# Optimization experiments

Measured on AMD Instinct MI355X. Metric: run time of the kernel, lower is better.

The kernel has to match this reference:

```python
import jax, jax.numpy as jnp
import numpy as np

N = 4096
DIMS = {"word": 768, "pos": 64, "liwc": 93, "entity": 256, "text": 768}
HID, OUT = 256, 128
VIEWS = ["word", "pos", "liwc", "entity", "text"]


def setup_inputs() -> dict:
    key = jax.random.key(0)
    inp = {}
    for i, v in enumerate(VIEWS):
        ka, kx, k1, k2 = jax.random.split(jax.random.fold_in(key, i), 4)
        d = DIMS[v]
        # dense row-normalized adjacency surrogate
        a = jax.random.uniform(ka, (N, N), dtype=jnp.float32)
        inp[f"adj_{v}"] = a / jnp.sum(a, axis=1, keepdims=True)
        inp[f"x_{v}"] = jax.random.normal(kx, (N, d), dtype=jnp.float32)
        inp[f"W1_{v}"] = jax.random.normal(k1, (d, HID), dtype=jnp.float32) * (2.0 / (d + HID)) ** 0.5
        inp[f"b1_{v}"] = jnp.zeros((HID,), dtype=jnp.float32)
        inp[f"W2_{v}"] = jax.random.normal(k2, (HID, OUT), dtype=jnp.float32) * (2.0 / (HID + OUT)) ** 0.5
        inp[f"b2_{v}"] = jnp.zeros((OUT,), dtype=jnp.float32)
    return inp


def _gcn2(adj, x, W1, b1, W2, b2):
    # layer 1: adj @ (x @ W1) + b1, relu (dropout is identity in eval mode)
    h = jax.nn.relu(adj @ (x @ W1) + b1)
    # layer 2
    return adj @ (h @ W2) + b2


def reference(adj_word, adj_pos, adj_liwc, adj_entity, adj_text,
              x_word, x_pos, x_liwc, x_entity, x_text,
              W1_word, b1_word, W2_word, b2_word,
              W1_pos, b1_pos, W2_pos, b2_pos,
              W1_liwc, b1_liwc, W2_liwc, b2_liwc,
              W1_entity, b1_entity, W2_entity, b2_entity,
              W1_text, b1_text, W2_text, b2_text):
    return (
        _gcn2(adj_word, x_word, W1_word, b1_word, W2_word, b2_word),
        _gcn2(adj_pos, x_pos, W1_pos, b1_pos, W2_pos, b2_pos),
        _gcn2(adj_liwc, x_liwc, W1_liwc, b1_liwc, W2_liwc, b2_liwc),
        _gcn2(adj_entity, x_entity, W1_entity, b1_entity, W2_entity, b2_entity),
        _gcn2(adj_text, x_text, W1_text, b1_text, W2_text, b2_text),
    )
```

## Files before the change

kernel.cpp:

```cpp
#include <hip/hip_runtime.h>
#include <stdint.h>

typedef unsigned short u16;
typedef __attribute__((ext_vector_type(8))) __bf16 bf16x8;
typedef __attribute__((ext_vector_type(4))) float f32x4;
typedef __attribute__((ext_vector_type(4))) u16 u16x4;
typedef __attribute__((ext_vector_type(8))) u16 u16x8;

#define BM 128
#define BN 128
#define BK 32
#define MTOT 4096

__device__ __forceinline__ u16 f2bf(float f) {
  union { float f; uint32_t u; } x; x.f = f;
  uint32_t r = x.u + 0x7FFFu + ((x.u >> 16) & 1u);
  return (u16)(r >> 16);
}
__device__ __forceinline__ float bf2f(u16 h) {
  union { uint32_t u; float f; } x; x.u = ((uint32_t)h) << 16;
  return x.f;
}

__device__ __forceinline__ void gload16(const void* g, void* lds) {
  __builtin_amdgcn_global_load_lds(
      (const __attribute__((address_space(1))) void*)g,
      (__attribute__((address_space(3))) void*)lds, 16, 0, 0);
}

struct ViewParams {
  const void* A;
  const u16* BT;
  void* C;
  const float* bias;
  int ldab, lda, N;
  int kspan;
  size_t partStride;
};
struct Params5 { ViewParams v[5]; };

template <int FLAGS, bool AF32, bool CF32>
__global__ __launch_bounds__(256) void gemm_kernel(Params5 p, int tilesPerView,
                                                   int ntiles, int kchunks) {
  constexpr int ABYTES = AF32 ? (BM * BK * 4) : (BM * BK * 2);
  __shared__ __align__(16) char smem[ABYTES + BN * BK * 2];
  u16* Bs = (u16*)(smem + ABYTES);

  const int bid = blockIdx.x;
  const int view = bid / tilesPerView;
  const int t = bid - view * tilesPerView;
  const int kc = t % kchunks;
  const int t2 = t / kchunks;
  const int nt = t2 % ntiles;
  const int mt = t2 / ntiles;
  ViewParams vp = p.v[view];
  const int ldab = vp.ldab, lda = vp.lda, N = vp.N;
  const int m0 = mt * BM, n0 = nt * BN;
  const int kbase = kc * vp.kspan;

  const int tid = threadIdx.x;
  const int wave = tid >> 6;
  const int lane = tid & 63;

  const int srow = lane >> 2;
  const int slot4 = lane & 3;
  const int rB0 = wave * 32 + srow;
  const int rB1 = rB0 + 16;
  const int cB0 = slot4 ^ ((rB0 >> 1) & 3);
  const int cB1 = slot4 ^ ((rB1 >> 1) & 3);
  const u16* gB0 = vp.BT + (size_t)(n0 + rB0) * ldab + kbase + cB0 * 8;
  const u16* gB1 = vp.BT + (size_t)(n0 + rB1) * ldab + kbase + cB1 * 8;
  u16* lB0 = Bs + (wave * 32) * 32;
  u16* lB1 = Bs + (wave * 32 + 16) * 32;

  const float* gAf[4];
  float* lAf[4];
  const u16 *gAb0 = nullptr, *gAb1 = nullptr;
  u16 *lAb0 = nullptr, *lAb1 = nullptr;
  if constexpr (AF32) {
    const float* Af = (const float*)vp.A;
    const int arow = lane >> 3;
    const int slot8 = lane & 7;
#pragma unroll
    for (int i = 0; i < 4; i++) {
      int r = wave * 32 + i * 8 + arow;
      int c = slot8 ^ (r & 7);
      gAf[i] = Af + (size_t)(m0 + r) * lda + kbase + c * 4;
      lAf[i] = (float*)smem + (wave * 32 + i * 8) * 32;
    }
  } else {
    const u16* Ab = (const u16*)vp.A;
    const int rA0 = wave * 32 + srow;
    const int rA1 = rA0 + 16;
    const int cA0 = slot4 ^ ((rA0 >> 1) & 3);
    const int cA1 = slot4 ^ ((rA1 >> 1) & 3);
    gAb0 = Ab + (size_t)(m0 + rA0) * lda + kbase + cA0 * 8;
    gAb1 = Ab + (size_t)(m0 + rA1) * lda + kbase + cA1 * 8;
    lAb0 = (u16*)smem + (wave * 32) * 32;
    lAb1 = (u16*)smem + (wave * 32 + 16) * 32;
  }

  const int lm = lane & 15;
  const int q = lane >> 4;
  const int wm = (wave >> 1) * 64;
  const int wn = (wave & 1) * 64;
  int aoff0[4], aoff1[4], boff[4];
#pragma unroll
  for (int i = 0; i < 4; i++) {
    int ml = wm + i * 16 + lm;
    if constexpr (AF32) {
      aoff0[i] = ml * 32 + ((2 * q) ^ (ml & 7)) * 4;
      aoff1[i] = ml * 32 + ((2 * q + 1) ^ (ml & 7)) * 4;
    } else {
      aoff0[i] = ml * 32 + (q ^ ((ml >> 1) & 3)) * 8;
    }
    int nl = wn + i * 16 + lm;
    boff[i] = nl * 32 + (q ^ ((nl >> 1) & 3)) * 8;
  }

  f32x4 acc[4][4];
#pragma unroll
  for (int i = 0; i < 4; i++)
#pragma unroll
    for (int j = 0; j < 4; j++) acc[i][j] = 0.0f;

  for (int ks = 0; ks < vp.kspan; ks += BK) {
    if constexpr (AF32) {
#pragma unroll
      for (int i = 0; i < 4; i++) { gload16(gAf[i], lAf[i]); gAf[i] += BK; }
    } else {
      gload16(gAb0, lAb0); gload16(gAb1, lAb1);
      gAb0 += BK; gAb1 += BK;
    }
    gload16(gB0, lB0); gload16(gB1, lB1);
    gB0 += BK; gB1 += BK;
    __syncthreads();

    bf16x8 af[4], bfr[4];
#pragma unroll
    for (int i = 0; i < 4; i++) {
      if constexpr (AF32) {
        f32x4 lo = *(const f32x4*)((const float*)smem + aoff0[i]);
        f32x4 hi = *(const f32x4*)((const float*)smem + aoff1[i]);
        bf16x8 a;
#pragma unroll
        for (int tt = 0; tt < 4; tt++) { a[tt] = (__bf16)lo[tt]; a[tt + 4] = (__bf16)hi[tt]; }
        af[i] = a;
      } else {
        af[i] = *(const bf16x8*)((const u16*)smem + aoff0[i]);
      }
    }
#pragma unroll
    for (int j = 0; j < 4; j++) bfr[j] = *(const bf16x8*)(Bs + boff[j]);
#pragma unroll
    for (int i = 0; i < 4; i++)
#pragma unroll
      for (int j = 0; j < 4; j++)
        acc[i][j] = __builtin_amdgcn_mfma_f32_16x16x32_bf16(af[i], bfr[j], acc[i][j], 0, 0, 0);
    __syncthreads();
  }

#pragma unroll
  for (int j = 0; j < 4; j++) {
    const int n = n0 + wn + j * 16 + lm;
    float bv = 0.0f;
    if (FLAGS & 2) bv = vp.bias[n];
#pragma unroll
    for (int i = 0; i < 4; i++) {
      const int mb = m0 + wm + i * 16 + q * 4;
      float v0 = acc[i][j][0], v1 = acc[i][j][1], v2 = acc[i][j][2], v3 = acc[i][j][3];
      if (FLAGS & 2) { v0 += bv; v1 += bv; v2 += bv; v3 += bv; }
      if (FLAGS & 4) {
        v0 = fmaxf(v0, 0.0f); v1 = fmaxf(v1, 0.0f);
        v2 = fmaxf(v2, 0.0f); v3 = fmaxf(v3, 0.0f);
      }
      if constexpr ((FLAGS & 1) != 0) {
        u16x4 pk;
        pk[0] = f2bf(v0); pk[1] = f2bf(v1); pk[2] = f2bf(v2); pk[3] = f2bf(v3);
        *(u16x4*)((u16*)vp.C + (size_t)kc * vp.partStride + (size_t)n * MTOT + mb) = pk;
      } else if constexpr (CF32) {
        float* cp = (float*)vp.C + (size_t)kc * vp.partStride + (size_t)mb * N + n;
        cp[0] = v0; cp[N] = v1; cp[2 * N] = v2; cp[3 * N] = v3;
      } else {
        u16* cp = (u16*)vp.C + (size_t)kc * vp.partStride + (size_t)mb * N + n;
        cp[0] = f2bf(v0); cp[N] = f2bf(v1); cp[2 * N] = f2bf(v2); cp[3 * N] = f2bf(v3);
      }
    }
  }
}

struct CombParams { const u16* parts; u16* out; const float* b[5]; int kchunks; };
__global__ __launch_bounds__(256) void comb_h_kernel(CombParams cp) {
  int idx = blockIdx.x * 256 + threadIdx.x;
  int v = idx >> 17;
  int e = (idx & 131071) << 3;
  float acc[8] = {0, 0, 0, 0, 0, 0, 0, 0};
  for (int kc = 0; kc < cp.kchunks; kc++) {
    u16x8 t = *(const u16x8*)(cp.parts + (((size_t)(kc * 5 + v)) << 20) + e);
#pragma unroll
    for (int j = 0; j < 8; j++) acc[j] += bf2f(t[j]);
  }
  const float* bp = cp.b[v] + (e & 255);
  u16x8 o;
#pragma unroll
  for (int j = 0; j < 8; j++) o[j] = f2bf(fmaxf(acc[j] + bp[j], 0.0f));
  *(u16x8*)(cp.out + (((size_t)v) << 20) + e) = o;
}

struct CombFParams { const float* parts; float* out; const float* b[5]; int kchunks; };
__global__ __launch_bounds__(256) void combf_kernel(CombFParams cp) {
  int idx = blockIdx.x * 256 + threadIdx.x;
  int v = idx >> 16;
  int e = (idx & 65535) << 3;
  float acc[8] = {0, 0, 0, 0, 0, 0, 0, 0};
  for (int kc = 0; kc < cp.kchunks; kc++) {
    const float* pp = cp.parts + (((size_t)(kc * 5 + v)) << 19) + e;
    f32x4 a = *(const f32x4*)pp;
    f32x4 b = *(const f32x4*)(pp + 4);
#pragma unroll
    for (int j = 0; j < 4; j++) { acc[j] += a[j]; acc[j + 4] += b[j]; }
  }
  const float* bp = cp.b[v] + (e & 127);
  f32x4 o0, o1;
#pragma unroll
  for (int j = 0; j < 4; j++) { o0[j] = acc[j] + bp[j]; o1[j] = acc[j + 4] + bp[j + 4]; }
  float* op = cp.out + (((size_t)v) << 19) + e;
  *(f32x4*)op = o0;
  *(f32x4*)(op + 4) = o1;
}

struct PrepParams {
  const float* W1[5]; u16* W1T[5];
  const float* W2[5]; u16* W2T[5];
  const float* xl; float* xlp;
  int d[5]; int Kp[5];
};

__global__ void prep_kernel(PrepParams p, int total) {
  int idx = blockIdx.x * 256 + threadIdx.x;
  if (idx >= total) return;
  int off = 0;
#pragma unroll
  for (int v = 0; v < 5; v++) {
    int sz = 256 * p.Kp[v];
    if (idx < off + sz) {
      int r = idx - off;
      int n = r / p.Kp[v];
      int k = r - n * p.Kp[v];
      p.W1T[v][r] = (k < p.d[v]) ? f2bf(p.W1[v][(size_t)k * 256 + n]) : (u16)0;
      return;
    }
    off += sz;
  }
#pragma unroll
  for (int v = 0; v < 5; v++) {
    if (idx < off + 128 * 256) {
      int r = idx - off;
      int n = r >> 8, k = r & 255;
      p.W2T[v][r] = f2bf(p.W2[v][(size_t)k * 128 + n]);
      return;
    }
    off += 128 * 256;
  }
  {
    int r = idx - off;
    int m = r / 96, k = r - m * 96;
    p.xlp[r] = (k < 93) ? p.xl[(size_t)m * 93 + k] : 0.0f;
  }
}

extern "C" void kernel_launch(void* const* d_in, const int* in_sizes, int n_in,
                              void* d_out, int out_size, void* d_ws, size_t ws_size,
                              hipStream_t stream) {
  (void)in_sizes; (void)n_in; (void)out_size;
  static const int dims[5] = {768, 64, 93, 256, 768};
  static const int Kp[5]   = {768, 64, 96, 256, 768};

  const float *adjf[5], *xf[5], *W1f[5], *b1f[5], *W2f[5], *b2f[5];
  for (int v = 0; v < 5; v++) {
    adjf[v] = (const float*)d_in[6 * v + 0];
    xf[v]   = (const float*)d_in[6 * v + 1];
    W1f[v]  = (const float*)d_in[6 * v + 2];
    b1f[v]  = (const float*)d_in[6 * v + 3];
    W2f[v]  = (const float*)d_in[6 * v + 4];
    b2f[v]  = (const float*)d_in[6 * v + 5];
  }

  const size_t VIEW = (size_t)256 * 4096;
  const size_t TV   = (size_t)128 * 4096;
  char* ws = (char*)d_ws;
  size_t off = 0;
  auto carve = [&](size_t bytes) { char* pp = ws + off; off += (bytes + 15) & ~(size_t)15; return pp; };
  u16* W1T[5]; for (int v = 0; v < 5; v++) W1T[v] = (u16*)carve((size_t)256 * Kp[v] * 2);
  u16* W2T[5]; for (int v = 0; v < 5; v++) W2T[v] = (u16*)carve((size_t)128 * 256 * 2);
  float* xlp = (float*)carve((size_t)4096 * 96 * 4);
  u16* Y1T = (u16*)carve(5 * VIEW * 2);
  u16* PARTS = (u16*)carve(2 * 5 * VIEW * 2);
  u16* HT = (u16*)carve(5 * VIEW * 2);
  const bool ksplit = ws_size >= off;
  u16* TT = Y1T;
  float* PARTSF = (float*)PARTS;

  PrepParams pp;
  int prepTot = 0;
  for (int v = 0; v < 5; v++) {
    pp.W1[v] = W1f[v]; pp.W1T[v] = W1T[v];
    pp.W2[v] = W2f[v]; pp.W2T[v] = W2T[v];
    pp.d[v] = dims[v]; pp.Kp[v] = Kp[v];
    prepTot += 256 * Kp[v];
  }
  pp.xl = xf[2]; pp.xlp = xlp;
  prepTot += 5 * 128 * 256 + 4096 * 96;
  prep_kernel<<<(prepTot + 255) / 256, 256, 0, stream>>>(pp, prepTot);

  Params5 pa;
  for (int v = 0; v < 5; v++)
    pa.v[v] = ViewParams{ (v == 2 ? (const void*)xlp : (const void*)xf[v]), W1T[v], Y1T + v * VIEW,
                          nullptr, Kp[v], Kp[v], 256, Kp[v], 0 };
  gemm_kernel<1, true, false><<<320, 256, 0, stream>>>(pa, 64, 2, 1);

  if (ksplit) {
    Params5 pb;
    for (int v = 0; v < 5; v++)
      pb.v[v] = ViewParams{ adjf[v], Y1T + v * VIEW, PARTS + v * VIEW,
                            nullptr, 4096, 4096, 256, 2048, 5 * VIEW };
    gemm_kernel<0, true, false><<<640, 256, 0, stream>>>(pb, 128, 2, 2);

    CombParams c1{ PARTS, HT, { b1f[0], b1f[1], b1f[2], b1f[3], b1f[4] }, 2 };
    comb_h_kernel<<<2560, 256, 0, stream>>>(c1);

    Params5 pc;
    for (int v = 0; v < 5; v++)
      pc.v[v] = ViewParams{ HT + v * VIEW, W2T[v], TT + v * TV,
                            nullptr, 256, 256, 128, 256, 0 };
    gemm_kernel<1, false, false><<<160, 256, 0, stream>>>(pc, 32, 1, 1);

    Params5 pd;
    for (int v = 0; v < 5; v++)
      pd.v[v] = ViewParams{ adjf[v], TT + v * TV, PARTSF + v * TV,
                            nullptr, 4096, 4096, 128, 2048, 5 * TV };
    gemm_kernel<0, true, true><<<320, 256, 0, stream>>>(pd, 64, 1, 2);

    CombFParams c2{ PARTSF, (float*)d_out, { b2f[0], b2f[1], b2f[2], b2f[3], b2f[4] }, 2 };
    combf_kernel<<<1280, 256, 0, stream>>>(c2);
  } else {
    Params5 pb;
    for (int v = 0; v < 5; v++)
      pb.v[v] = ViewParams{ adjf[v], Y1T + v * VIEW, HT + v * VIEW,
                            b1f[v], 4096, 4096, 256, 4096, 0 };
    gemm_kernel<6, true, false><<<320, 256, 0, stream>>>(pb, 64, 2, 1);

    Params5 pc;
    for (int v = 0; v < 5; v++)
      pc.v[v] = ViewParams{ HT + v * VIEW, W2T[v], TT + v * TV,
                            nullptr, 256, 256, 128, 256, 0 };
    gemm_kernel<1, false, false><<<160, 256, 0, stream>>>(pc, 32, 1, 1);

    Params5 pd;
    float* outp = (float*)d_out;
    for (int v = 0; v < 5; v++)
      pd.v[v] = ViewParams{ adjf[v], TT + v * TV, outp + v * TV,
                            b2f[v], 4096, 4096, 128, 4096, 0 };
    gemm_kernel<2, true, true><<<160, 256, 0, stream>>>(pd, 32, 1, 1);
  }
}
```

Measured before the change: 579.4 us.

## Double-buffer LDS tiles to overlap global loads with MFMA compute

Doubles the shared-memory footprint into two ping-pong buffers, so the next K-slice is issued with async global-to-LDS loads while MFMAs run on the current slice. This removes one of the two barriers per iteration and hides part of the global load latency behind compute. In exchange LDS use doubles, which may lower occupancy, especially for the fp32-A variant. It also depends on the barrier correctly covering completion of the async direct-to-LDS loads.

```diff
diff --git a/kernel.cpp b/kernel.cpp
--- a/kernel.cpp
+++ b/kernel.cpp
@@ -43,8 +43,8 @@
 __global__ __launch_bounds__(256) void gemm_kernel(Params5 p, int tilesPerView,
                                                    int ntiles, int kchunks) {
   constexpr int ABYTES = AF32 ? (BM * BK * 4) : (BM * BK * 2);
-  __shared__ __align__(16) char smem[ABYTES + BN * BK * 2];
-  u16* Bs = (u16*)(smem + ABYTES);
+  constexpr int BUFB = ABYTES + BN * BK * 2;
+  __shared__ __align__(16) char smem[2 * BUFB];
 
   const int bid = blockIdx.x;
   const int view = bid / tilesPerView;
@@ -70,13 +70,12 @@
   const int cB1 = slot4 ^ ((rB1 >> 1) & 3);
   const u16* gB0 = vp.BT + (size_t)(n0 + rB0) * ldab + kbase + cB0 * 8;
   const u16* gB1 = vp.BT + (size_t)(n0 + rB1) * ldab + kbase + cB1 * 8;
-  u16* lB0 = Bs + (wave * 32) * 32;
-  u16* lB1 = Bs + (wave * 32 + 16) * 32;
+  const int lB0_off = ABYTES + (wave * 32) * 32 * 2;
+  const int lB1_off = ABYTES + (wave * 32 + 16) * 32 * 2;
 
   const float* gAf[4];
-  float* lAf[4];
   const u16 *gAb0 = nullptr, *gAb1 = nullptr;
-  u16 *lAb0 = nullptr, *lAb1 = nullptr;
+  int lA_off[4];
   if constexpr (AF32) {
     const float* Af = (const float*)vp.A;
     const int arow = lane >> 3;
@@ -86,7 +85,7 @@
       int r = wave * 32 + i * 8 + arow;
       int c = slot8 ^ (r & 7);
       gAf[i] = Af + (size_t)(m0 + r) * lda + kbase + c * 4;
-      lAf[i] = (float*)smem + (wave * 32 + i * 8) * 32;
+      lA_off[i] = (wave * 32 + i * 8) * 32 * 4;
     }
   } else {
     const u16* Ab = (const u16*)vp.A;
@@ -96,8 +95,8 @@
     const int cA1 = slot4 ^ ((rA1 >> 1) & 3);
     gAb0 = Ab + (size_t)(m0 + rA0) * lda + kbase + cA0 * 8;
     gAb1 = Ab + (size_t)(m0 + rA1) * lda + kbase + cA1 * 8;
-    lAb0 = (u16*)smem + (wave * 32) * 32;
-    lAb1 = (u16*)smem + (wave * 32 + 16) * 32;
+    lA_off[0] = (wave * 32) * 32 * 2;
+    lA_off[1] = (wave * 32 + 16) * 32 * 2;
   }
 
   const int lm = lane & 15;
@@ -124,32 +123,36 @@
 #pragma unroll
     for (int j = 0; j < 4; j++) acc[i][j] = 0.0f;
 
-  for (int ks = 0; ks < vp.kspan; ks += BK) {
+  auto stage = [&](char* bufp) {
     if constexpr (AF32) {
 #pragma unroll
-      for (int i = 0; i < 4; i++) { gload16(gAf[i], lAf[i]); gAf[i] += BK; }
+      for (int i = 0; i < 4; i++) { gload16(gAf[i], bufp + lA_off[i]); gAf[i] += BK; }
     } else {
-      gload16(gAb0, lAb0); gload16(gAb1, lAb1);
+      gload16(gAb0, bufp + lA_off[0]);
+      gload16(gAb1, bufp + lA_off[1]);
       gAb0 += BK; gAb1 += BK;
     }
-    gload16(gB0, lB0); gload16(gB1, lB1);
+    gload16(gB0, bufp + lB0_off);
+    gload16(gB1, bufp + lB1_off);
     gB0 += BK; gB1 += BK;
-    __syncthreads();
-
+  };
+
+  auto compute = [&](const char* bufp) {
     bf16x8 af[4], bfr[4];
 #pragma unroll
     for (int i = 0; i < 4; i++) {
       if constexpr (AF32) {
-        f32x4 lo = *(const f32x4*)((const float*)smem + aoff0[i]);
-        f32x4 hi = *(const f32x4*)((const float*)smem + aoff1[i]);
+        f32x4 lo = *(const f32x4*)((const float*)bufp + aoff0[i]);
+        f32x4 hi = *(const f32x4*)((const float*)bufp + aoff1[i]);
         bf16x8 a;
 #pragma unroll
         for (int tt = 0; tt < 4; tt++) { a[tt] = (__bf16)lo[tt]; a[tt + 4] = (__bf16)hi[tt]; }
         af[i] = a;
       } else {
-        af[i] = *(const bf16x8*)((const u16*)smem + aoff0[i]);
+        af[i] = *(const bf16x8*)((const u16*)bufp + aoff0[i]);
       }
     }
+    const u16* Bs = (const u16*)(bufp + ABYTES);
 #pragma unroll
     for (int j = 0; j < 4; j++) bfr[j] = *(const bf16x8*)(Bs + boff[j]);
 #pragma unroll
@@ -157,8 +160,20 @@
 #pragma unroll
       for (int j = 0; j < 4; j++)
         acc[i][j] = __builtin_amdgcn_mfma_f32_16x16x32_bf16(af[i], bfr[j], acc[i][j], 0, 0, 0);
+  };
+
+  char* curp = smem;
+  char* nxtp = smem + BUFB;
+  stage(curp);
+  __syncthreads();
+  const int nsteps = vp.kspan / BK;
+  for (int s = 0; s < nsteps - 1; s++) {
+    stage(nxtp);
+    compute(curp);
     __syncthreads();
-  }
+    char* tmp = curp; curp = nxtp; nxtp = tmp;
+  }
+  compute(curp);
 
 #pragma unroll
   for (int j = 0; j < 4; j++) {
```

New measurement: 574.2 us. About the same (-0.9%).
